# Optimization experiments

Hardware: AMD Instinct MI355X
Metric: run time of the kernel (lower is better)

The kernel has to match this reference:

```python
import jax, jax.numpy as jnp
import numpy as np

EMBED_DIM = 512
NUM_HEADS = 8
HEAD_DIM = EMBED_DIM // NUM_HEADS
BATCH = 2
SEQ = 4096
LN_EPS = 1e-5


def setup_inputs() -> dict:
    key = jax.random.key(0)
    ks = jax.random.split(key, 10)
    s = 1.0 / np.sqrt(EMBED_DIM)
    d = dict(
        x=jax.random.normal(ks[0], (BATCH, SEQ, EMBED_DIM), dtype=jnp.float32),
        wq=jax.random.normal(ks[1], (EMBED_DIM, EMBED_DIM), dtype=jnp.float32) * s,
        bq=jnp.zeros((EMBED_DIM,), jnp.float32),
        wk=jax.random.normal(ks[2], (EMBED_DIM, EMBED_DIM), dtype=jnp.float32) * s,
        bk=jnp.zeros((EMBED_DIM,), jnp.float32),
        wv=jax.random.normal(ks[3], (EMBED_DIM, EMBED_DIM), dtype=jnp.float32) * s,
        bv=jnp.zeros((EMBED_DIM,), jnp.float32),
        wo=jax.random.normal(ks[4], (EMBED_DIM, EMBED_DIM), dtype=jnp.float32) * s,
        bo=jnp.zeros((EMBED_DIM,), jnp.float32),
        ln_g=jnp.ones((EMBED_DIM,), jnp.float32),
        ln_b=jnp.zeros((EMBED_DIM,), jnp.float32),
    )
    return d


def reference(x, wq, bq, wk, bk, wv, bv, wo, bo, ln_g, ln_b):
    B, S, E = x.shape
    H, D = NUM_HEADS, HEAD_DIM
    residual = x
    # QKV projections (weights stored [in, out])
    q = (x @ wq + bq).reshape(B, S, H, D).transpose(0, 2, 1, 3)  # [B,H,S,D]
    k = (x @ wk + bk).reshape(B, S, H, D).transpose(0, 2, 1, 3)
    v = (x @ wv + bv).reshape(B, S, H, D).transpose(0, 2, 1, 3)
    # scaled dot-product attention
    scores = jnp.einsum('bhsd,bhtd->bhst', q, k) / jnp.sqrt(jnp.float32(D))
    attn = jax.nn.softmax(scores, axis=-1)
    ctx = jnp.einsum('bhst,bhtd->bhsd', attn, v)  # [B,H,S,D]
    ctx = ctx.transpose(0, 2, 1, 3).reshape(B, S, E)
    # output projection (dropout=0 in eval) + residual + LayerNorm
    out = ctx @ wo + bo
    y = out + residual
    mu = jnp.mean(y, axis=-1, keepdims=True)
    var = jnp.var(y, axis=-1, keepdims=True)
    y = (y - mu) * jax.lax.rsqrt(var + LN_EPS) * ln_g + ln_b
    return y
```

## Files before the change

kernel.cpp:

```cpp
#include <hip/hip_runtime.h>


typedef unsigned short u16;
typedef unsigned int u32;
typedef short bf16x8 __attribute__((ext_vector_type(8)));
typedef float f32x2 __attribute__((ext_vector_type(2)));
typedef float f32x4 __attribute__((ext_vector_type(4)));
typedef float f32x8 __attribute__((ext_vector_type(8)));
typedef float f32x16 __attribute__((ext_vector_type(16)));
typedef unsigned short u16x4 __attribute__((ext_vector_type(4)));
typedef unsigned int u32x2 __attribute__((ext_vector_type(2)));
typedef unsigned int u32x4 __attribute__((ext_vector_type(4)));

#define S_LEN 4096
#define E_DIM 512
#define H_NUM 8
#define D_DIM 64
#define M_ROWS 8192

#define Q_SCALE 0.18033688011112042f

static __device__ __forceinline__ u16 f2bf(float f) {
    unsigned int u = __float_as_uint(f);
    u += 0x7fffu + ((u >> 16) & 1u);
    return (u16)(u >> 16);
}

static __device__ __forceinline__ u32 cvt_pk_bf16(float a, float b) {
    u32 r;
    asm("v_cvt_pk_bf16_f32 %0, %1, %2" : "=v"(r) : "v"(a), "v"(b));
    return r;
}

#if __has_builtin(__builtin_amdgcn_exp2f)
#define EXP2(x) __builtin_amdgcn_exp2f(x)
#else
static __device__ __forceinline__ float exp2_hw(float x) {
    float r;
    asm volatile("v_exp_f32 %0, %1\n\ts_nop 1" : "=v"(r) : "v"(x));
    return r;
}
#define EXP2(x) exp2_hw(x)
#endif

static __device__ __forceinline__ float vsum16(f32x16 v) {
    f32x8 a = __builtin_shufflevector(v, v, 0, 1, 2, 3, 4, 5, 6, 7) +
              __builtin_shufflevector(v, v, 8, 9, 10, 11, 12, 13, 14, 15);
    f32x4 b = __builtin_shufflevector(a, a, 0, 1, 2, 3) +
              __builtin_shufflevector(a, a, 4, 5, 6, 7);
    f32x2 c = __builtin_shufflevector(b, b, 0, 1) +
              __builtin_shufflevector(b, b, 2, 3);
    return c[0] + c[1];
}

static __device__ __forceinline__ void gload_lds16(const u16* g, u16* l) {
    __builtin_amdgcn_global_load_lds(
        (const __attribute__((address_space(1))) u32*)g,
        (__attribute__((address_space(3))) u32*)l, 16, 0, 0);
}

__global__ __launch_bounds__(256) void cvt_k(const float* __restrict__ src,
                                             u16* __restrict__ dst, int n4) {
    int i = blockIdx.x * 256 + threadIdx.x;
    if (i >= n4) return;
    float4 v = ((const float4*)src)[i];
    u16x4 o;
    o[0] = f2bf(v.x); o[1] = f2bf(v.y); o[2] = f2bf(v.z); o[3] = f2bf(v.w);
    ((u16x4*)dst)[i] = o;
}

__global__ __launch_bounds__(256) void cvtT4_k(
    const float* __restrict__ w0, const float* __restrict__ w1,
    const float* __restrict__ w2, const float* __restrict__ w3,
    u16* __restrict__ o0, u16* __restrict__ o1,
    u16* __restrict__ o2, u16* __restrict__ o3)
{
    __shared__ float fT[64][68];
    const int g = blockIdx.x;
    const int which = g >> 6;
    const int tile = g & 63;
    const int k0 = (tile >> 3) * 64, n0 = (tile & 7) * 64;
    const float* w = which == 0 ? w0 : which == 1 ? w1 : which == 2 ? w2 : w3;
    u16* o = which == 0 ? o0 : which == 1 ? o1 : which == 2 ? o2 : o3;
    const int tr = threadIdx.x >> 4, tc = threadIdx.x & 15;
    #pragma unroll
    for (int p = 0; p < 4; p++) {
        const int kr = p * 16 + tr;
        float4 v = *(const float4*)&w[(size_t)(k0 + kr) * 512 + n0 + tc * 4];
        fT[tc * 4 + 0][kr] = v.x;
        fT[tc * 4 + 1][kr] = v.y;
        fT[tc * 4 + 2][kr] = v.z;
        fT[tc * 4 + 3][kr] = v.w;
    }
    __syncthreads();
    #pragma unroll
    for (int p = 0; p < 4; p++) {
        const int nr = p * 16 + tr;
        u16x4 ov;
        ov[0] = f2bf(fT[nr][tc * 4 + 0]);
        ov[1] = f2bf(fT[nr][tc * 4 + 1]);
        ov[2] = f2bf(fT[nr][tc * 4 + 2]);
        ov[3] = f2bf(fT[nr][tc * 4 + 3]);
        *(u16x4*)&o[(size_t)(n0 + nr) * 512 + k0 + tc * 4] = ov;
    }
}

template <int BM, int BN, int MODE>
__global__ __launch_bounds__(256) void gemm_k(
    const u16* __restrict__ A,
    const u16* __restrict__ Wt0, const u16* __restrict__ Wt1,
    const u16* __restrict__ Wt2,
    const float* __restrict__ b0, const float* __restrict__ b1,
    const float* __restrict__ b2,
    u16* __restrict__ q_out, u16* __restrict__ k_out, u16* __restrict__ vt_out,
    const float* __restrict__ resid, float* __restrict__ of32)
{
    constexpr int FM = BM / 32, FN = BN / 32;
    __shared__ __align__(16) u16 Asm[BM * 32];
    __shared__ __align__(16) u16 Bsm[BN * 32];

    const int t = threadIdx.x, wave = t >> 6, lane = t & 63;
    constexpr int nb_per = 512 / BN;
    int sel, bn;
    if (MODE == 0) { sel = blockIdx.x / nb_per; bn = blockIdx.x % nb_per; }
    else           { sel = 0;                   bn = blockIdx.x; }
    const int bm = blockIdx.y;

    const u16* Wt = (MODE == 0) ? (sel == 0 ? Wt0 : (sel == 1 ? Wt1 : Wt2)) : Wt0;
    const float* bias = (MODE == 0) ? (sel == 0 ? b0 : (sel == 1 ? b1 : b2)) : b0;

    const int wm = (wave >> 1) * (BM / 2);
    const int wn = (wave & 1) * (BN / 2);
    const int lrow = lane & 15, kq = (lane >> 4) * 8;

    f32x4 acc[FM][FN];
    #pragma unroll
    for (int i = 0; i < FM; i++)
        #pragma unroll
        for (int j = 0; j < FN; j++)
            acc[i][j] = (f32x4){0.f, 0.f, 0.f, 0.f};

    const u16* Ag = A + (size_t)bm * BM * 512 + (size_t)(t >> 2) * 512 + (t & 3) * 8;
    const u16* Bg = Wt + (size_t)bn * BN * 512 + (size_t)(t >> 2) * 512 + (t & 3) * 8;
    u16* Al = Asm + (size_t)wave * 512;
    u16* Bl = Bsm + (size_t)wave * 512;

    for (int kk = 0; kk < 512; kk += 32) {
        #pragma unroll
        for (int p = 0; p < BM / 32; p++)
            gload_lds16(Ag + (size_t)p * 64 * 512 + kk, Al + p * 2048);
        #pragma unroll
        for (int p = 0; p < BN / 32; p++)
            gload_lds16(Bg + (size_t)p * 64 * 512 + kk, Bl + p * 2048);
        __syncthreads();

        bf16x8 af[FM], bfv[FN];
        #pragma unroll
        for (int i = 0; i < FM; i++)
            af[i] = *(const bf16x8*)&Asm[(wm + i * 16 + lrow) * 32 + kq];
        #pragma unroll
        for (int j = 0; j < FN; j++)
            bfv[j] = *(const bf16x8*)&Bsm[(wn + j * 16 + lrow) * 32 + kq];
        #pragma unroll
        for (int i = 0; i < FM; i++)
            #pragma unroll
            for (int j = 0; j < FN; j++)
                acc[i][j] = __builtin_amdgcn_mfma_f32_16x16x32_bf16(
                    af[i], bfv[j], acc[i][j], 0, 0, 0);
        __syncthreads();
    }

    #pragma unroll
    for (int i = 0; i < FM; i++) {
        #pragma unroll
        for (int j = 0; j < FN; j++) {
            const int col = bn * BN + wn + j * 16 + lrow;
            const float bcol = bias[col];
            const int row0 = bm * BM + wm + i * 16 + (lane >> 4) * 4;
            if (MODE == 0) {
                const int b = row0 >> 12, s0v = row0 & 4095;
                const int h = col >> 6,  d = col & 63;
                if (sel == 2) {
                    u16x4 pk;
                    #pragma unroll
                    for (int q = 0; q < 4; q++)
                        pk[q] = f2bf(acc[i][j][q] + bcol);
                    *(u16x4*)&vt_out[(((size_t)(b * 8 + h)) * 64 + d) * 4096 + s0v] = pk;
                } else {
                    u16* o = (sel == 0) ? q_out : k_out;
                    const float sc = (sel == 0) ? Q_SCALE : 1.0f;
                    #pragma unroll
                    for (int q = 0; q < 4; q++)
                        o[(((size_t)(b * 8 + h)) * 4096 + s0v + q) * 64 + d] =
                            f2bf((acc[i][j][q] + bcol) * sc);
                }
            } else {
                #pragma unroll
                for (int q = 0; q < 4; q++) {
                    const size_t idx = (size_t)(row0 + q) * 512 + col;
                    of32[idx] = acc[i][j][q] + bcol + resid[idx];
                }
            }
        }
    }
}

__global__ __launch_bounds__(512, 2) void attn_k(
    const u16* __restrict__ Q, const u16* __restrict__ K,
    const u16* __restrict__ Vt, u16* __restrict__ ctx)
{
    __shared__ __align__(16) u16 SM[32768];

    const int t = threadIdx.x, w = t >> 6, lane = t & 63;
    const int l31 = lane & 31, hi = lane >> 5;
    const int kh = w >> 2, wl = w & 3;

    const int bid = blockIdx.x;
    const int xcd = bid & 7, j = bid >> 3;
    const int head = xcd * 2 + (j & 1);
    const int qt = j >> 1;

    const u16* Qb = Q + (size_t)head * S_LEN * D_DIM;
    const u16* Kb = K + (size_t)head * S_LEN * D_DIM;
    const u16* Vb = Vt + (size_t)head * D_DIM * S_LEN;
    const int q0w = qt * 256 + wl * 64;

    bf16x8 qfA[4], qfB[4];
    #pragma unroll
    for (int ks = 0; ks < 4; ks++) {
        qfA[ks] = *(const bf16x8*)&Qb[(size_t)(q0w + l31) * 64 + ks * 16 + hi * 8];
        qfB[ks] = *(const bf16x8*)&Qb[(size_t)(q0w + 32 + l31) * 64 + ks * 16 + hi * 8];
    }

    u16* const KH = SM + kh * 16384;
    u16* const VH = KH + 8192;

    const u16* kp[8];
    const u16* vp[8];
    #pragma unroll
    for (int i = 0; i < 8; i++) {
        const int r = (i >> 2) * 32 + l31;
        const int c = (i & 3) * 2 + hi;
        const int phys = r * 8 + (c ^ (r & 7));
        kp[i] = KH + phys * 8;
        vp[i] = VH + phys * 8;
    }

    f32x16 acc0A = {0.f}, acc1A = {0.f}, acc0B = {0.f}, acc1B = {0.f};
    float lA = 0.f, lB = 0.f;

    const int th = t & 255;
    const int c0 = th, c1 = th + 256;
    const int sr0 = c0 >> 3, sc0 = (c0 & 7) ^ (sr0 & 7);
    const int sr1 = c1 >> 3, sc1 = (c1 & 7) ^ (sr1 & 7);
    const u16* kg0 = Kb + (size_t)(kh * 2048 + sr0) * 64 + sc0 * 8;
    const u16* kg1 = Kb + (size_t)(kh * 2048 + sr1) * 64 + sc1 * 8;
    const u16* vg0 = Vb + (size_t)sr0 * S_LEN + kh * 2048 + sc0 * 8;
    const u16* vg1 = Vb + (size_t)sr1 * S_LEN + kh * 2048 + sc1 * 8;
    u16* const kd0 = KH + wl * 512;
    u16* const kd1 = KH + 2048 + wl * 512;
    u16* const vd0 = VH + wl * 512;
    u16* const vd1 = VH + 2048 + wl * 512;

#define ATTN_STAGE(DST)                                                      \
    {                                                                        \
        gload_lds16(kg0, kd0 + (DST)); gload_lds16(kg1, kd1 + (DST));        \
        gload_lds16(vg0, vd0 + (DST)); gload_lds16(vg1, vd1 + (DST));        \
        kg0 += 4096; kg1 += 4096; vg0 += 64; vg1 += 64;                      \
    }

#define ATTN_COMPUTE(BUF)                                                    \
    {                                                                        \
        f32x16 sA0 = {0.f}, sA1 = {0.f}, sB0 = {0.f}, sB1 = {0.f};           \
        __builtin_amdgcn_s_setprio(1);                                       \
        _Pragma("unroll")                                                    \
        for (int ks = 0; ks < 4; ks++) {                                     \
            bf16x8 ka = *(const bf16x8*)(kp[ks] + (BUF));                    \
            bf16x8 kb2 = *(const bf16x8*)(kp[4 + ks] + (BUF));               \
            sA0 = __builtin_amdgcn_mfma_f32_32x32x16_bf16(ka, qfA[ks], sA0, 0, 0, 0); \
            sB0 = __builtin_amdgcn_mfma_f32_32x32x16_bf16(ka, qfB[ks], sB0, 0, 0, 0); \
            sA1 = __builtin_amdgcn_mfma_f32_32x32x16_bf16(kb2, qfA[ks], sA1, 0, 0, 0); \
            sB1 = __builtin_amdgcn_mfma_f32_32x32x16_bf16(kb2, qfB[ks], sB1, 0, 0, 0); \
        }                                                                    \
        __builtin_amdgcn_s_setprio(0);                                       \
        _Pragma("unroll")                                                    \
        for (int e = 0; e < 16; e++) {                                       \
            sA0[e] = EXP2(sA0[e]); sA1[e] = EXP2(sA1[e]);                    \
            sB0[e] = EXP2(sB0[e]); sB1[e] = EXP2(sB1[e]);                    \
        }                                                                    \
        lA += vsum16(sA0 + sA1);                                             \
        lB += vsum16(sB0 + sB1);                                             \
        bf16x8 pfA[4], pfB[4];                                               \
        _Pragma("unroll")                                                    \
        for (int ks = 0; ks < 4; ks++) {                                     \
            const int r0 = (ks & 1) * 8;                                     \
            const f32x16& sa = (ks < 2) ? sA0 : sA1;                         \
            u32 ax1 = cvt_pk_bf16(sa[r0 + 0], sa[r0 + 1]);                   \
            u32 ay1 = cvt_pk_bf16(sa[r0 + 4], sa[r0 + 5]);                   \
            asm("v_permlane32_swap_b32 %0, %1" : "+v"(ax1), "+v"(ay1));      \
            u32 ax2 = cvt_pk_bf16(sa[r0 + 2], sa[r0 + 3]);                   \
            u32 ay2 = cvt_pk_bf16(sa[r0 + 6], sa[r0 + 7]);                   \
            asm("v_permlane32_swap_b32 %0, %1" : "+v"(ax2), "+v"(ay2));      \
            u32x4 wva; wva[0] = ax1; wva[1] = ax2; wva[2] = ay1; wva[3] = ay2; \
            pfA[ks] = *(bf16x8*)&wva;                                        \
            const f32x16& sb = (ks < 2) ? sB0 : sB1;                         \
            u32 bx1 = cvt_pk_bf16(sb[r0 + 0], sb[r0 + 1]);                   \
            u32 by1 = cvt_pk_bf16(sb[r0 + 4], sb[r0 + 5]);                   \
            asm("v_permlane32_swap_b32 %0, %1" : "+v"(bx1), "+v"(by1));      \
            u32 bx2 = cvt_pk_bf16(sb[r0 + 2], sb[r0 + 3]);                   \
            u32 by2 = cvt_pk_bf16(sb[r0 + 6], sb[r0 + 7]);                   \
            asm("v_permlane32_swap_b32 %0, %1" : "+v"(bx2), "+v"(by2));      \
            u32x4 wvb; wvb[0] = bx1; wvb[1] = bx2; wvb[2] = by1; wvb[3] = by2; \
            pfB[ks] = *(bf16x8*)&wvb;                                        \
        }                                                                    \
        __builtin_amdgcn_s_setprio(1);                                       \
        _Pragma("unroll")                                                    \
        for (int ks = 0; ks < 4; ks++) {                                     \
            bf16x8 va = *(const bf16x8*)(vp[ks] + (BUF));                    \
            bf16x8 vb2 = *(const bf16x8*)(vp[4 + ks] + (BUF));               \
            acc0A = __builtin_amdgcn_mfma_f32_32x32x16_bf16(va, pfA[ks], acc0A, 0, 0, 0); \
            acc0B = __builtin_amdgcn_mfma_f32_32x32x16_bf16(va, pfB[ks], acc0B, 0, 0, 0); \
            acc1A = __builtin_amdgcn_mfma_f32_32x32x16_bf16(vb2, pfA[ks], acc1A, 0, 0, 0); \
            acc1B = __builtin_amdgcn_mfma_f32_32x32x16_bf16(vb2, pfB[ks], acc1B, 0, 0, 0); \
        }                                                                    \
        __builtin_amdgcn_s_setprio(0);                                       \
    }

    ATTN_STAGE(0);
    __syncthreads();

    for (int it = 0; it < 16; ++it) {
        ATTN_STAGE(4096);
        ATTN_COMPUTE(0);
        __syncthreads();
        if (it != 15) ATTN_STAGE(0);
        ATTN_COMPUTE(4096);
        __syncthreads();
    }

    __syncthreads();
    float* const cb = (float*)SM;
    float* const p = cb + (size_t)(wl * 64 + lane) * 34;
    if (kh == 1) {
        #pragma unroll
        for (int e = 0; e < 16; e++) { p[e] = acc0A[e]; p[16 + e] = acc0B[e]; }
        p[32] = lA; p[33] = lB;
    }
    __syncthreads();
    if (kh == 0) {
        #pragma unroll
        for (int e = 0; e < 16; e++) { acc0A[e] += p[e]; acc0B[e] += p[16 + e]; }
        lA += p[32]; lB += p[33];
    }
    __syncthreads();
    if (kh == 1) {
        #pragma unroll
        for (int e = 0; e < 16; e++) { p[e] = acc1A[e]; p[16 + e] = acc1B[e]; }
    }
    __syncthreads();
    if (kh == 0) {
        #pragma unroll
        for (int e = 0; e < 16; e++) { acc1A[e] += p[e]; acc1B[e] += p[16 + e]; }
        lA += __shfl_xor(lA, 32);
        lB += __shfl_xor(lB, 32);

        const int b = head >> 3, h = head & 7;
        const float liA = 1.0f / lA, liB = 1.0f / lB;
        const size_t oA = (size_t)(b * S_LEN + q0w + l31) * 512 + h * 64 + 4 * hi;
        const size_t oB = oA + (size_t)32 * 512;
        #pragma unroll
        for (int rq = 0; rq < 4; rq++) {
            u32x2 wa;
            wa[0] = cvt_pk_bf16(acc0A[4 * rq + 0] * liA, acc0A[4 * rq + 1] * liA);
            wa[1] = cvt_pk_bf16(acc0A[4 * rq + 2] * liA, acc0A[4 * rq + 3] * liA);
            *(u32x2*)&ctx[oA + 8 * rq] = wa;
            wa[0] = cvt_pk_bf16(acc1A[4 * rq + 0] * liA, acc1A[4 * rq + 1] * liA);
            wa[1] = cvt_pk_bf16(acc1A[4 * rq + 2] * liA, acc1A[4 * rq + 3] * liA);
            *(u32x2*)&ctx[oA + 32 + 8 * rq] = wa;
            wa[0] = cvt_pk_bf16(acc0B[4 * rq + 0] * liB, acc0B[4 * rq + 1] * liB);
            wa[1] = cvt_pk_bf16(acc0B[4 * rq + 2] * liB, acc0B[4 * rq + 3] * liB);
            *(u32x2*)&ctx[oB + 8 * rq] = wa;
            wa[0] = cvt_pk_bf16(acc1B[4 * rq + 0] * liB, acc1B[4 * rq + 1] * liB);
            wa[1] = cvt_pk_bf16(acc1B[4 * rq + 2] * liB, acc1B[4 * rq + 3] * liB);
            *(u32x2*)&ctx[oB + 32 + 8 * rq] = wa;
        }
    }
#undef ATTN_STAGE
#undef ATTN_COMPUTE
}

__global__ __launch_bounds__(256) void ln_k(const float* __restrict__ y,
                                            const float* __restrict__ g,
                                            const float* __restrict__ beta,
                                            float* __restrict__ out)
{
    const int w = threadIdx.x >> 6, lane = threadIdx.x & 63;
    const size_t row = (size_t)blockIdx.x * 4 + w;
    const float4* yr = (const float4*)(y + row * 512);
    float4 a = yr[lane], b = yr[lane + 64];
    float s  = a.x + a.y + a.z + a.w + b.x + b.y + b.z + b.w;
    float ss = a.x*a.x + a.y*a.y + a.z*a.z + a.w*a.w
             + b.x*b.x + b.y*b.y + b.z*b.z + b.w*b.w;
    #pragma unroll
    for (int o = 1; o < 64; o <<= 1) {
        s  += __shfl_xor(s, o);
        ss += __shfl_xor(ss, o);
    }
    const float mu  = s * (1.0f / 512.0f);
    const float var = ss * (1.0f / 512.0f) - mu * mu;
    const float inv = rsqrtf(var + 1e-5f);
    const float4* g4 = (const float4*)g;
    const float4* b4 = (const float4*)beta;
    float4 ga = g4[lane], gb = g4[lane + 64];
    float4 ba = b4[lane], bb = b4[lane + 64];
    float4 oa, ob;
    oa.x = (a.x - mu) * inv * ga.x + ba.x;
    oa.y = (a.y - mu) * inv * ga.y + ba.y;
    oa.z = (a.z - mu) * inv * ga.z + ba.z;
    oa.w = (a.w - mu) * inv * ga.w + ba.w;
    ob.x = (b.x - mu) * inv * gb.x + bb.x;
    ob.y = (b.y - mu) * inv * gb.y + bb.y;
    ob.z = (b.z - mu) * inv * gb.z + bb.z;
    ob.w = (b.w - mu) * inv * gb.w + bb.w;
    float4* orow = (float4*)(out + row * 512);
    orow[lane] = oa;
    orow[lane + 64] = ob;
}

extern "C" void kernel_launch(void* const* d_in, const int* in_sizes, int n_in,
                              void* d_out, int out_size, void* d_ws, size_t ws_size,
                              hipStream_t stream)
{
    const float* x    = (const float*)d_in[0];
    const float* wq   = (const float*)d_in[1];
    const float* bq   = (const float*)d_in[2];
    const float* wk   = (const float*)d_in[3];
    const float* bk   = (const float*)d_in[4];
    const float* wv   = (const float*)d_in[5];
    const float* bv   = (const float*)d_in[6];
    const float* wo   = (const float*)d_in[7];
    const float* bo   = (const float*)d_in[8];
    const float* ln_g = (const float*)d_in[9];
    const float* ln_b = (const float*)d_in[10];

    char* ws = (char*)d_ws;
    u16* xb   = (u16*)(ws);
    u16* wqt  = (u16*)(ws + 8388608);
    u16* wkt  = (u16*)(ws + 8912896);
    u16* wvt  = (u16*)(ws + 9437184);
    u16* wot  = (u16*)(ws + 9961472);
    u16* Qb   = (u16*)(ws + 10485760);
    u16* Kb   = (u16*)(ws + 18874368);
    u16* Vtb  = (u16*)(ws + 27262976);
    u16* ctxb = (u16*)(ws + 35651584);
    float* yb = (float*)(ws + 10485760);

    cvt_k<<<4096, 256, 0, stream>>>(x, xb, (M_ROWS * E_DIM) / 4);
    cvtT4_k<<<256, 256, 0, stream>>>(wq, wk, wv, wo, wqt, wkt, wvt, wot);

    gemm_k<128, 128, 0><<<dim3(12, 64), 256, 0, stream>>>(
        xb, wqt, wkt, wvt, bq, bk, bv, Qb, Kb, Vtb, nullptr, nullptr);

    attn_k<<<256, 512, 0, stream>>>(Qb, Kb, Vtb, ctxb);

    gemm_k<128, 64, 2><<<dim3(8, 64), 256, 0, stream>>>(
        ctxb, wot, wot, wot, bo, bo, bo, nullptr, nullptr, nullptr, x, yb);

    ln_k<<<2048, 256, 0, stream>>>(yb, ln_g, ln_b, (float*)d_out);
}
```

Baseline: 150.9 us.

## Software-pipeline attention QK/softmax/PV halves and merge conversion kernels

Splits the attention inner step into two 32-key halves so that the QK MFMA of one half overlaps the exp/pack of the other and the PV MFMAs. The QK of the next tile's first half is issued right after the barrier, giving a cross-iteration pipeline. This aims to hide the exp and convert latency behind matrix work. It also fuses the x conversion and weight-transpose kernels into one launch to save a kernel launch. The cost is more live registers, which could lower occupancy or cause spills.

```diff
diff --git a/kernel.cpp b/kernel.cpp
--- a/kernel.cpp
+++ b/kernel.cpp
@@ -59,24 +59,23 @@
         (__attribute__((address_space(3))) u32*)l, 16, 0, 0);
 }
 
-__global__ __launch_bounds__(256) void cvt_k(const float* __restrict__ src,
-                                             u16* __restrict__ dst, int n4) {
-    int i = blockIdx.x * 256 + threadIdx.x;
-    if (i >= n4) return;
-    float4 v = ((const float4*)src)[i];
-    u16x4 o;
-    o[0] = f2bf(v.x); o[1] = f2bf(v.y); o[2] = f2bf(v.z); o[3] = f2bf(v.w);
-    ((u16x4*)dst)[i] = o;
-}
-
-__global__ __launch_bounds__(256) void cvtT4_k(
+__global__ __launch_bounds__(256) void cvt_all_k(
+    const float* __restrict__ x, u16* __restrict__ xb,
     const float* __restrict__ w0, const float* __restrict__ w1,
     const float* __restrict__ w2, const float* __restrict__ w3,
     u16* __restrict__ o0, u16* __restrict__ o1,
     u16* __restrict__ o2, u16* __restrict__ o3)
 {
     __shared__ float fT[64][68];
-    const int g = blockIdx.x;
+    if (blockIdx.x < 4096) {
+        int i = blockIdx.x * 256 + threadIdx.x;
+        float4 v = ((const float4*)x)[i];
+        u16x4 o;
+        o[0] = f2bf(v.x); o[1] = f2bf(v.y); o[2] = f2bf(v.z); o[3] = f2bf(v.w);
+        ((u16x4*)xb)[i] = o;
+        return;
+    }
+    const int g = blockIdx.x - 4096;
     const int which = g >> 6;
     const int tile = g & 63;
     const int k0 = (tile >> 3) * 64, n0 = (tile & 7) * 64;
@@ -248,6 +247,8 @@
 
     f32x16 acc0A = {0.f}, acc1A = {0.f}, acc0B = {0.f}, acc1B = {0.f};
     float lA = 0.f, lB = 0.f;
+    f32x16 sCA, sCB, sNA, sNB;
+    bf16x8 pfA[2], pfB[2];
 
     const int th = t & 255;
     const int c0 = th, c1 = th + 256;
@@ -269,74 +270,86 @@
         kg0 += 4096; kg1 += 4096; vg0 += 64; vg1 += 64;                      \
     }
 
-#define ATTN_COMPUTE(BUF)                                                    \
+#define QK_H(BUF, H, SA, SB)                                                 \
     {                                                                        \
-        f32x16 sA0 = {0.f}, sA1 = {0.f}, sB0 = {0.f}, sB1 = {0.f};           \
+        SA = (f32x16){0.f}; SB = (f32x16){0.f};                              \
         __builtin_amdgcn_s_setprio(1);                                       \
         _Pragma("unroll")                                                    \
         for (int ks = 0; ks < 4; ks++) {                                     \
-            bf16x8 ka = *(const bf16x8*)(kp[ks] + (BUF));                    \
-            bf16x8 kb2 = *(const bf16x8*)(kp[4 + ks] + (BUF));               \
-            sA0 = __builtin_amdgcn_mfma_f32_32x32x16_bf16(ka, qfA[ks], sA0, 0, 0, 0); \
-            sB0 = __builtin_amdgcn_mfma_f32_32x32x16_bf16(ka, qfB[ks], sB0, 0, 0, 0); \
-            sA1 = __builtin_amdgcn_mfma_f32_32x32x16_bf16(kb2, qfA[ks], sA1, 0, 0, 0); \
-            sB1 = __builtin_amdgcn_mfma_f32_32x32x16_bf16(kb2, qfB[ks], sB1, 0, 0, 0); \
+            bf16x8 ka = *(const bf16x8*)(kp[4 * (H) + ks] + (BUF));          \
+            SA = __builtin_amdgcn_mfma_f32_32x32x16_bf16(ka, qfA[ks], SA, 0, 0, 0); \
+            SB = __builtin_amdgcn_mfma_f32_32x32x16_bf16(ka, qfB[ks], SB, 0, 0, 0); \
         }                                                                    \
         __builtin_amdgcn_s_setprio(0);                                       \
+    }
+
+#define EXPPACK_H(SA, SB)                                                    \
+    {                                                                        \
         _Pragma("unroll")                                                    \
         for (int e = 0; e < 16; e++) {                                       \
-            sA0[e] = EXP2(sA0[e]); sA1[e] = EXP2(sA1[e]);                    \
-            sB0[e] = EXP2(sB0[e]); sB1[e] = EXP2(sB1[e]);                    \
+            SA[e] = EXP2(SA[e]); SB[e] = EXP2(SB[e]);                        \
         }                                                                    \
-        lA += vsum16(sA0 + sA1);                                             \
-        lB += vsum16(sB0 + sB1);                                             \
-        bf16x8 pfA[4], pfB[4];                                               \
+        lA += vsum16(SA);                                                    \
+        lB += vsum16(SB);                                                    \
         _Pragma("unroll")                                                    \
-        for (int ks = 0; ks < 4; ks++) {                                     \
-            const int r0 = (ks & 1) * 8;                                     \
-            const f32x16& sa = (ks < 2) ? sA0 : sA1;                         \
-            u32 ax1 = cvt_pk_bf16(sa[r0 + 0], sa[r0 + 1]);                   \
-            u32 ay1 = cvt_pk_bf16(sa[r0 + 4], sa[r0 + 5]);                   \
+        for (int jx = 0; jx < 2; jx++) {                                     \
+            const int r0 = jx * 8;                                           \
+            u32 ax1 = cvt_pk_bf16(SA[r0 + 0], SA[r0 + 1]);                   \
+            u32 ay1 = cvt_pk_bf16(SA[r0 + 4], SA[r0 + 5]);                   \
             asm("v_permlane32_swap_b32 %0, %1" : "+v"(ax1), "+v"(ay1));      \
-            u32 ax2 = cvt_pk_bf16(sa[r0 + 2], sa[r0 + 3]);                   \
-            u32 ay2 = cvt_pk_bf16(sa[r0 + 6], sa[r0 + 7]);                   \
+            u32 ax2 = cvt_pk_bf16(SA[r0 + 2], SA[r0 + 3]);                   \
+            u32 ay2 = cvt_pk_bf16(SA[r0 + 6], SA[r0 + 7]);                   \
             asm("v_permlane32_swap_b32 %0, %1" : "+v"(ax2), "+v"(ay2));      \
             u32x4 wva; wva[0] = ax1; wva[1] = ax2; wva[2] = ay1; wva[3] = ay2; \
-            pfA[ks] = *(bf16x8*)&wva;                                        \
-            const f32x16& sb = (ks < 2) ? sB0 : sB1;                         \
-            u32 bx1 = cvt_pk_bf16(sb[r0 + 0], sb[r0 + 1]);                   \
-            u32 by1 = cvt_pk_bf16(sb[r0 + 4], sb[r0 + 5]);                   \
+            pfA[jx] = *(bf16x8*)&wva;                                        \
+            u32 bx1 = cvt_pk_bf16(SB[r0 + 0], SB[r0 + 1]);                   \
+            u32 by1 = cvt_pk_bf16(SB[r0 + 4], SB[r0 + 5]);                   \
             asm("v_permlane32_swap_b32 %0, %1" : "+v"(bx1), "+v"(by1));      \
-            u32 bx2 = cvt_pk_bf16(sb[r0 + 2], sb[r0 + 3]);                   \
-            u32 by2 = cvt_pk_bf16(sb[r0 + 6], sb[r0 + 7]);                   \
+            u32 bx2 = cvt_pk_bf16(SB[r0 + 2], SB[r0 + 3]);                   \
+            u32 by2 = cvt_pk_bf16(SB[r0 + 6], SB[r0 + 7]);                   \
             asm("v_permlane32_swap_b32 %0, %1" : "+v"(bx2), "+v"(by2));      \
             u32x4 wvb; wvb[0] = bx1; wvb[1] = bx2; wvb[2] = by1; wvb[3] = by2; \
-            pfB[ks] = *(bf16x8*)&wvb;                                        \
+            pfB[jx] = *(bf16x8*)&wvb;                                        \
         }                                                                    \
+    }
+
+#define PV_H(BUF, H)                                                         \
+    {                                                                        \
         __builtin_amdgcn_s_setprio(1);                                       \
         _Pragma("unroll")                                                    \
-        for (int ks = 0; ks < 4; ks++) {                                     \
-            bf16x8 va = *(const bf16x8*)(vp[ks] + (BUF));                    \
-            bf16x8 vb2 = *(const bf16x8*)(vp[4 + ks] + (BUF));               \
-            acc0A = __builtin_amdgcn_mfma_f32_32x32x16_bf16(va, pfA[ks], acc0A, 0, 0, 0); \
-            acc0B = __builtin_amdgcn_mfma_f32_32x32x16_bf16(va, pfB[ks], acc0B, 0, 0, 0); \
-            acc1A = __builtin_amdgcn_mfma_f32_32x32x16_bf16(vb2, pfA[ks], acc1A, 0, 0, 0); \
-            acc1B = __builtin_amdgcn_mfma_f32_32x32x16_bf16(vb2, pfB[ks], acc1B, 0, 0, 0); \
+        for (int jx = 0; jx < 2; jx++) {                                     \
+            bf16x8 va = *(const bf16x8*)(vp[2 * (H) + jx] + (BUF));          \
+            bf16x8 vb2 = *(const bf16x8*)(vp[4 + 2 * (H) + jx] + (BUF));     \
+            acc0A = __builtin_amdgcn_mfma_f32_32x32x16_bf16(va, pfA[jx], acc0A, 0, 0, 0); \
+            acc0B = __builtin_amdgcn_mfma_f32_32x32x16_bf16(va, pfB[jx], acc0B, 0, 0, 0); \
+            acc1A = __builtin_amdgcn_mfma_f32_32x32x16_bf16(vb2, pfA[jx], acc1A, 0, 0, 0); \
+            acc1B = __builtin_amdgcn_mfma_f32_32x32x16_bf16(vb2, pfB[jx], acc1B, 0, 0, 0); \
         }                                                                    \
         __builtin_amdgcn_s_setprio(0);                                       \
     }
 
+#define BODY(BUF, NBUF, LAST)                                                \
+    {                                                                        \
+        if (!(LAST)) ATTN_STAGE(NBUF);                                       \
+        QK_H(BUF, 1, sNA, sNB);                                              \
+        EXPPACK_H(sCA, sCB);                                                 \
+        PV_H(BUF, 0);                                                        \
+        EXPPACK_H(sNA, sNB);                                                 \
+        PV_H(BUF, 1);                                                        \
+        __syncthreads();                                                     \
+        if (!(LAST)) QK_H(NBUF, 0, sCA, sCB);                                \
+    }
+
     ATTN_STAGE(0);
     __syncthreads();
-
-    for (int it = 0; it < 16; ++it) {
-        ATTN_STAGE(4096);
-        ATTN_COMPUTE(0);
-        __syncthreads();
-        if (it != 15) ATTN_STAGE(0);
-        ATTN_COMPUTE(4096);
-        __syncthreads();
-    }
+    QK_H(0, 0, sCA, sCB);
+
+    for (int it = 0; it < 15; ++it) {
+        BODY(0, 4096, 0);
+        BODY(4096, 0, 0);
+    }
+    BODY(0, 4096, 0);
+    BODY(4096, 0, 1);
 
     __syncthreads();
     float* const cb = (float*)SM;
@@ -386,7 +399,10 @@
         }
     }
 #undef ATTN_STAGE
-#undef ATTN_COMPUTE
+#undef QK_H
+#undef EXPPACK_H
+#undef PV_H
+#undef BODY
 }
 
 __global__ __launch_bounds__(256) void ln_k(const float* __restrict__ y,
@@ -455,8 +471,8 @@
     u16* ctxb = (u16*)(ws + 35651584);
     float* yb = (float*)(ws + 10485760);
 
-    cvt_k<<<4096, 256, 0, stream>>>(x, xb, (M_ROWS * E_DIM) / 4);
-    cvtT4_k<<<256, 256, 0, stream>>>(wq, wk, wv, wo, wqt, wkt, wvt, wot);
+    cvt_all_k<<<4352, 256, 0, stream>>>(x, xb, wq, wk, wv, wo,
+                                        wqt, wkt, wvt, wot);
 
     gemm_k<128, 128, 0><<<dim3(12, 64), 256, 0, stream>>>(
         xb, wqt, wkt, wvt, bq, bk, bv, Qb, Kb, Vtb, nullptr, nullptr);
```

After: 149.7 us. No clear change (-0.8%).
